# Kernel tuning notes

Measured on AMD Instinct MI355X. Metric: run time of the kernel, lower is better.

Reference implementation:

```python
import jax, jax.numpy as jnp
import numpy as np

N = 1_000_000
HID = 128

def setup_inputs() -> dict:
    key = jax.random.key(0)
    ks = jax.random.split(key, 4)
    F = jnp.eye(2, dtype=jnp.float32)[None] + 0.1 * jax.random.normal(ks[0], (N, 2, 2), dtype=jnp.float32)
    W1 = jax.random.normal(ks[1], (7, HID), dtype=jnp.float32) * (1.0 / np.sqrt(7))
    b1 = jnp.zeros((HID,), dtype=jnp.float32)
    W2 = jax.random.normal(ks[2], (HID, HID), dtype=jnp.float32) * (1.0 / np.sqrt(HID))
    b2 = jnp.zeros((HID,), dtype=jnp.float32)
    W3 = jax.random.normal(ks[3], (HID, 4), dtype=jnp.float32) * (1.0 / np.sqrt(HID))
    b3 = jnp.zeros((4,), dtype=jnp.float32)
    return {"F": F, "W1": W1, "b1": b1, "W2": W2, "b2": b2, "W3": W3, "b3": b3}

def reference(F, W1, b1, W2, b2, W3, b3):
    F = F.reshape(-1, 2, 2)                      # [N,2,2]
    U, sigma, Vh = jnp.linalg.svd(F)             # batched 2x2 SVD
    R = jnp.matmul(U, Vh)                        # rotation part, [N,2,2]
    FtF = jnp.einsum('nij,nik->njk', F, F)       # F^T F, [N,2,2]
    I = jnp.eye(2, dtype=F.dtype)
    I1 = sigma - 1.0                             # [N,2]
    I2 = (FtF - I).reshape(-1, 4)                # [N,4]
    det = F[:, 0, 0] * F[:, 1, 1] - F[:, 0, 1] * F[:, 1, 0]
    I3 = det[:, None] - 1.0                      # [N,1]
    inv = jnp.concatenate([I1, I2, I3], axis=1)  # [N,7]
    h = jax.nn.relu(inv @ W1 + b1)
    h = jax.nn.relu(h @ W2 + b2)
    x = (h @ W3 + b3).reshape(-1, 2, 2)
    x = (x + jnp.swapaxes(x, 1, 2)) * 0.5        # symmetrize
    delta_Fp = jnp.matmul(R, x)
    return delta_Fp + F
```

## Files before the change

kernel.cpp:

```cpp
#include <hip/hip_runtime.h>

typedef _Float16 f16x8 __attribute__((ext_vector_type(8)));
typedef __fp16   fp16x2r __attribute__((ext_vector_type(2)));
typedef float    f32x4 __attribute__((ext_vector_type(4)));

#define MFMA(a, b, c) __builtin_amdgcn_mfma_f32_16x16x32_f16((a), (b), (c), 0, 0, 0)

__device__ inline f16x8 zero8() {
    f16x8 z;
#pragma unroll
    for (int i = 0; i < 8; ++i) z[i] = (_Float16)0.0f;
    return z;
}

__device__ inline f16x8 relu_pack8_rtn(f32x4 lo, f32x4 hi) {
    f16x8 v;
#pragma unroll
    for (int i = 0; i < 4; ++i) {
        v[i]     = (_Float16)fmaxf(lo[i], 0.f);
        v[i + 4] = (_Float16)fmaxf(hi[i], 0.f);
    }
    return v;
}

__device__ inline f16x8 relu_pack8_rtz(f32x4 lo, f32x4 hi) {
    const fp16x2r p0 = __builtin_amdgcn_cvt_pkrtz(fmaxf(lo[0], 0.f), fmaxf(lo[1], 0.f));
    const fp16x2r p1 = __builtin_amdgcn_cvt_pkrtz(fmaxf(lo[2], 0.f), fmaxf(lo[3], 0.f));
    const fp16x2r p2 = __builtin_amdgcn_cvt_pkrtz(fmaxf(hi[0], 0.f), fmaxf(hi[1], 0.f));
    const fp16x2r p3 = __builtin_amdgcn_cvt_pkrtz(fmaxf(hi[2], 0.f), fmaxf(hi[3], 0.f));
    uint4 u = { __builtin_bit_cast(unsigned int, p0), __builtin_bit_cast(unsigned int, p1),
                __builtin_bit_cast(unsigned int, p2), __builtin_bit_cast(unsigned int, p3) };
    return __builtin_bit_cast(f16x8, u);
}

__global__ __launch_bounds__(256, 1)
void DeformationCorrector_78967268704761_kernel(
        const float* __restrict__ F,
        const float* __restrict__ W1, const float* __restrict__ b1,
        const float* __restrict__ W2, const float* __restrict__ b2,
        const float* __restrict__ W3, const float* __restrict__ b3,
        float* __restrict__ out, int N)
{
    __shared__ __align__(16) _Float16 W2A[8][4][64][8];
    __shared__ __align__(16) _Float16 W1A[8][16][8];
    __shared__ __align__(16) _Float16 W3A[4][16][8];
    __shared__ __align__(16) float    b2L[128];
    __shared__ __align__(16) _Float16 invL[4][64][8];

    const int tid  = threadIdx.x;
    const int lane = tid & 63;
    const int w    = tid >> 6;
    const int l15  = tid & 15;
    const int quad = (tid >> 4) & 3;

    for (int m = tid; m < 128 * 128; m += 256) {
        const int k = m >> 7, n = m & 127;
        const int s = k >> 5, j = ((k >> 4) & 1) * 4 + (k & 3), q = (k >> 2) & 3;
        W2A[n >> 4][s][q * 16 + (n & 15)][j] = (_Float16)W2[m];
    }
    for (int f = tid; f < 1024; f += 256) {
        const int mt = f >> 7, n15 = (f >> 3) & 15, j = f & 7;
        W1A[mt][n15][j] = (_Float16)((j < 7) ? W1[j * 128 + mt * 16 + n15]
                                             : b1[mt * 16 + n15]);
    }
    for (int f = tid; f < 512; f += 256) {
        const int s3 = f >> 7, idx = (f >> 3) & 15, j = f & 7;
        const int q = idx >> 2, c3 = idx & 3;
        const int ch2 = (2 * s3 + (j >> 2)) * 16 + q * 4 + (j & 3);
        W3A[s3][idx][j] = (_Float16)W3[ch2 * 4 + c3];
    }
    if (tid < 128) b2L[tid] = b2[tid];
    f32x4 b3i;
    {
        const float4 t = *(const float4*)b3;
        b3i = (quad == 0) ? (f32x4){t.x, t.y, t.z, t.w} : (f32x4){0.f, 0.f, 0.f, 0.f};
    }
    __syncthreads();

    const int ntiles = (N + 255) >> 8;
    const int stride = (int)gridDim.x;

    float a, b, c, d;
    {
        const int p0 = blockIdx.x * 256 + tid;
        if (blockIdx.x < ntiles && p0 < N) {
            const float4 f4 = *(const float4*)(F + 4ll * p0);
            a = f4.x; b = f4.y; c = f4.z; d = f4.w;
        } else { a = 1.f; b = 0.f; c = 0.f; d = 1.f; }
    }

    for (int tile = blockIdx.x; tile < ntiles; tile += stride) {
        float na = 1.f, nb = 0.f, nc = 0.f, nd = 1.f;
        {
            const int pn = (tile + stride) * 256 + tid;
            if (tile + stride < ntiles && pn < N) {
                const float4 f4 = *(const float4*)(F + 4ll * pn);
                na = f4.x; nb = f4.y; nc = f4.z; nd = f4.w;
            }
        }
        const int p = tile * 256 + tid;

        const float x1 = a + d, y1 = c - b, x2 = a - d, y2 = c + b;
        const float h1v = sqrtf(x1 * x1 + y1 * y1);
        const float h2v = sqrtf(x2 * x2 + y2 * y2);
        const float s1 = 0.5f * (h1v + h2v), s2 = 0.5f * (h1v - h2v);
        const float ir = 1.0f / h1v;
        const float Rc = x1 * ir, Rs = y1 * ir;
        f16x8 iv;
        iv[0] = (_Float16)(s1 - 1.f);
        iv[1] = (_Float16)(s2 - 1.f);
        iv[2] = (_Float16)(a * a + c * c - 1.f);
        const float i3 = a * b + c * d;
        iv[3] = (_Float16)i3;
        iv[4] = (_Float16)i3;
        iv[5] = (_Float16)(b * b + d * d - 1.f);
        iv[6] = (_Float16)(a * d - b * c - 1.f);
        iv[7] = (_Float16)1.0f;
        *(f16x8*)(&invL[w][lane][0]) = iv;

        f16x8 B1[4];
#pragma unroll
        for (int nt = 0; nt < 4; ++nt)
            B1[nt] = (quad == 0) ? *(const f16x8*)(&invL[w][nt * 16 + l15][0]) : zero8();

        f16x8 B2[4][4];
#pragma unroll
        for (int s = 0; s < 4; ++s) {
            const f16x8 aLo = (quad == 0) ? *(const f16x8*)(&W1A[2 * s][l15][0])     : zero8();
            const f16x8 aHi = (quad == 0) ? *(const f16x8*)(&W1A[2 * s + 1][l15][0]) : zero8();
#pragma unroll
            for (int nt = 0; nt < 4; ++nt) {
                const f32x4 cz  = {0.f, 0.f, 0.f, 0.f};
                const f32x4 dLo = MFMA(aLo, B1[nt], cz);
                const f32x4 dHi = MFMA(aHi, B1[nt], cz);
                B2[s][nt] = relu_pack8_rtn(dLo, dHi);
            }
        }

        f32x4 acc3[4];
#pragma unroll
        for (int nt = 0; nt < 4; ++nt) acc3[nt] = b3i;

#pragma unroll
        for (int s3 = 0; s3 < 4; ++s3) {
            f32x4 accE[4], accO[4];
            {
                const f32x4 bvE = *(const f32x4*)(&b2L[(2 * s3) * 16 + quad * 4]);
                const f32x4 bvO = *(const f32x4*)(&b2L[(2 * s3 + 1) * 16 + quad * 4]);
#pragma unroll
                for (int nt = 0; nt < 4; ++nt) { accE[nt] = bvE; accO[nt] = bvO; }
            }
#pragma unroll
            for (int s = 0; s < 4; ++s) {
                const f16x8 aE = *(const f16x8*)(&W2A[2 * s3][s][lane][0]);
                const f16x8 aO = *(const f16x8*)(&W2A[2 * s3 + 1][s][lane][0]);
#pragma unroll
                for (int nt = 0; nt < 4; ++nt) {
                    accE[nt] = MFMA(aE, B2[s][nt], accE[nt]);
                    accO[nt] = MFMA(aO, B2[s][nt], accO[nt]);
                }
            }
            const f16x8 a3 = (l15 < 4) ? *(const f16x8*)(&W3A[s3][quad * 4 + l15][0]) : zero8();
#pragma unroll
            for (int nt = 0; nt < 4; ++nt) {
                const f16x8 b3f = relu_pack8_rtz(accE[nt], accO[nt]);
                acc3[nt] = MFMA(a3, b3f, acc3[nt]);
            }
        }

        if (quad == 0) {
#pragma unroll
            for (int nt = 0; nt < 4; ++nt)
                *(f16x8*)(&invL[w][nt * 16 + l15][0]) = __builtin_bit_cast(f16x8, acc3[nt]);
        }
        const f32x4 xv = __builtin_bit_cast(f32x4, *(const f16x8*)(&invL[w][lane][0]));
        const float xm  = 0.5f * (xv[1] + xv[2]);
        const float d00 = Rc * xv[0] - Rs * xm;
        const float d01 = Rc * xm    - Rs * xv[3];
        const float d10 = Rs * xv[0] + Rc * xm;
        const float d11 = Rs * xm    + Rc * xv[3];
        if (p < N) {
            float4 o;
            o.x = a + d00; o.y = b + d01; o.z = c + d10; o.w = d + d11;
            *(float4*)(out + 4ll * p) = o;
        }

        a = na; b = nb; c = nc; d = nd;
    }
}

extern "C" void kernel_launch(void* const* d_in, const int* in_sizes, int n_in,
                              void* d_out, int out_size, void* d_ws, size_t ws_size,
                              hipStream_t stream) {
    const float* F  = (const float*)d_in[0];
    const float* W1 = (const float*)d_in[1];
    const float* b1 = (const float*)d_in[2];
    const float* W2 = (const float*)d_in[3];
    const float* b2 = (const float*)d_in[4];
    const float* W3 = (const float*)d_in[5];
    const float* b3 = (const float*)d_in[6];
    float* out = (float*)d_out;
    const int N = in_sizes[0] / 4;
    const int ntiles = (N + 255) / 256;
    const int grid = ntiles < 512 ? ntiles : 512;
    DeformationCorrector_78967268704761_kernel<<<grid, 256, 0, stream>>>(
        F, W1, b1, W2, b2, W3, b3, out, N);
}
```

Baseline: 141.8 us.

## Process MLP per 16-point subtile in rolled loop and drop F prefetch

The per-wave MLP now loops over the four 16-point column groups with a non-unrolled loop instead of holding all four groups' activations and accumulators in registers at once, and the software prefetch of the next tile's F values is removed. The b3 bias moves into shared memory and is added after the last MFMA. This cuts register pressure, but it also cuts the independent MFMA chains available to hide latency, and W2 fragments are re-read from LDS four times per tile. With launch_bounds(256,1) and a fixed grid, occupancy may not rise, so the lost ILP and the lost load prefetch could dominate.

```diff
diff --git a/kernel.cpp b/kernel.cpp
--- a/kernel.cpp
+++ b/kernel.cpp
@@ -45,6 +45,7 @@
     __shared__ __align__(16) _Float16 W1A[8][16][8];
     __shared__ __align__(16) _Float16 W3A[4][16][8];
     __shared__ __align__(16) float    b2L[128];
+    __shared__ __align__(16) float    b3L[4];
     __shared__ __align__(16) _Float16 invL[4][64][8];
 
     const int tid  = threadIdx.x;
@@ -70,35 +71,20 @@
         W3A[s3][idx][j] = (_Float16)W3[ch2 * 4 + c3];
     }
     if (tid < 128) b2L[tid] = b2[tid];
-    f32x4 b3i;
-    {
-        const float4 t = *(const float4*)b3;
-        b3i = (quad == 0) ? (f32x4){t.x, t.y, t.z, t.w} : (f32x4){0.f, 0.f, 0.f, 0.f};
-    }
+    if (tid < 4)   b3L[tid] = b3[tid];
     __syncthreads();
 
     const int ntiles = (N + 255) >> 8;
     const int stride = (int)gridDim.x;
 
-    float a, b, c, d;
-    {
-        const int p0 = blockIdx.x * 256 + tid;
-        if (blockIdx.x < ntiles && p0 < N) {
-            const float4 f4 = *(const float4*)(F + 4ll * p0);
+    for (int tile = blockIdx.x; tile < ntiles; tile += stride) {
+        const int p = tile * 256 + tid;
+
+        float a, b, c, d;
+        if (p < N) {
+            const float4 f4 = *(const float4*)(F + 4ll * p);
             a = f4.x; b = f4.y; c = f4.z; d = f4.w;
         } else { a = 1.f; b = 0.f; c = 0.f; d = 1.f; }
-    }
-
-    for (int tile = blockIdx.x; tile < ntiles; tile += stride) {
-        float na = 1.f, nb = 0.f, nc = 0.f, nd = 1.f;
-        {
-            const int pn = (tile + stride) * 256 + tid;
-            if (tile + stride < ntiles && pn < N) {
-                const float4 f4 = *(const float4*)(F + 4ll * pn);
-                na = f4.x; nb = f4.y; nc = f4.z; nd = f4.w;
-            }
-        }
-        const int p = tile * 256 + tid;
 
         const float x1 = a + d, y1 = c - b, x2 = a - d, y2 = c + b;
         const float h1v = sqrtf(x1 * x1 + y1 * y1);
@@ -118,61 +104,46 @@
         iv[7] = (_Float16)1.0f;
         *(f16x8*)(&invL[w][lane][0]) = iv;
 
-        f16x8 B1[4];
+#pragma unroll 1
+        for (int q4 = 0; q4 < 4; ++q4) {
+            const f16x8 B1 = (quad == 0)
+                ? *(const f16x8*)(&invL[w][q4 * 16 + l15][0]) : zero8();
+
+            f16x8 B2[4];
 #pragma unroll
-        for (int nt = 0; nt < 4; ++nt)
-            B1[nt] = (quad == 0) ? *(const f16x8*)(&invL[w][nt * 16 + l15][0]) : zero8();
+            for (int s = 0; s < 4; ++s) {
+                const f16x8 aLo = (quad == 0) ? *(const f16x8*)(&W1A[2 * s][l15][0])     : zero8();
+                const f16x8 aHi = (quad == 0) ? *(const f16x8*)(&W1A[2 * s + 1][l15][0]) : zero8();
+                const f32x4 cz  = {0.f, 0.f, 0.f, 0.f};
+                const f32x4 dLo = MFMA(aLo, B1, cz);
+                const f32x4 dHi = MFMA(aHi, B1, cz);
+                B2[s] = relu_pack8_rtn(dLo, dHi);
+            }
 
-        f16x8 B2[4][4];
+            f32x4 acc3 = {0.f, 0.f, 0.f, 0.f};
 #pragma unroll
-        for (int s = 0; s < 4; ++s) {
-            const f16x8 aLo = (quad == 0) ? *(const f16x8*)(&W1A[2 * s][l15][0])     : zero8();
-            const f16x8 aHi = (quad == 0) ? *(const f16x8*)(&W1A[2 * s + 1][l15][0]) : zero8();
+            for (int s3 = 0; s3 < 4; ++s3) {
+                f32x4 accE = *(const f32x4*)(&b2L[(2 * s3) * 16 + quad * 4]);
+                f32x4 accO = *(const f32x4*)(&b2L[(2 * s3 + 1) * 16 + quad * 4]);
 #pragma unroll
-            for (int nt = 0; nt < 4; ++nt) {
-                const f32x4 cz  = {0.f, 0.f, 0.f, 0.f};
-                const f32x4 dLo = MFMA(aLo, B1[nt], cz);
-                const f32x4 dHi = MFMA(aHi, B1[nt], cz);
-                B2[s][nt] = relu_pack8_rtn(dLo, dHi);
+                for (int s = 0; s < 4; ++s) {
+                    const f16x8 aE = *(const f16x8*)(&W2A[2 * s3][s][lane][0]);
+                    const f16x8 aO = *(const f16x8*)(&W2A[2 * s3 + 1][s][lane][0]);
+                    accE = MFMA(aE, B2[s], accE);
+                    accO = MFMA(aO, B2[s], accO);
+                }
+                const f16x8 a3 = (l15 < 4) ? *(const f16x8*)(&W3A[s3][quad * 4 + l15][0]) : zero8();
+                const f16x8 b3f = relu_pack8_rtz(accE, accO);
+                acc3 = MFMA(a3, b3f, acc3);
+            }
+
+            if (quad == 0) {
+                const f32x4 b3v4 = *(const f32x4*)(&b3L[0]);
+                *(f16x8*)(&invL[w][q4 * 16 + l15][0]) =
+                    __builtin_bit_cast(f16x8, acc3 + b3v4);
             }
         }
 
-        f32x4 acc3[4];
-#pragma unroll
-        for (int nt = 0; nt < 4; ++nt) acc3[nt] = b3i;
-
-#pragma unroll
-        for (int s3 = 0; s3 < 4; ++s3) {
-            f32x4 accE[4], accO[4];
-            {
-                const f32x4 bvE = *(const f32x4*)(&b2L[(2 * s3) * 16 + quad * 4]);
-                const f32x4 bvO = *(const f32x4*)(&b2L[(2 * s3 + 1) * 16 + quad * 4]);
-#pragma unroll
-                for (int nt = 0; nt < 4; ++nt) { accE[nt] = bvE; accO[nt] = bvO; }
-            }
-#pragma unroll
-            for (int s = 0; s < 4; ++s) {
-                const f16x8 aE = *(const f16x8*)(&W2A[2 * s3][s][lane][0]);
-                const f16x8 aO = *(const f16x8*)(&W2A[2 * s3 + 1][s][lane][0]);
-#pragma unroll
-                for (int nt = 0; nt < 4; ++nt) {
-                    accE[nt] = MFMA(aE, B2[s][nt], accE[nt]);
-                    accO[nt] = MFMA(aO, B2[s][nt], accO[nt]);
-                }
-            }
-            const f16x8 a3 = (l15 < 4) ? *(const f16x8*)(&W3A[s3][quad * 4 + l15][0]) : zero8();
-#pragma unroll
-            for (int nt = 0; nt < 4; ++nt) {
-                const f16x8 b3f = relu_pack8_rtz(accE[nt], accO[nt]);
-                acc3[nt] = MFMA(a3, b3f, acc3[nt]);
-            }
-        }
-
-        if (quad == 0) {
-#pragma unroll
-            for (int nt = 0; nt < 4; ++nt)
-                *(f16x8*)(&invL[w][nt * 16 + l15][0]) = __builtin_bit_cast(f16x8, acc3[nt]);
-        }
         const f32x4 xv = __builtin_bit_cast(f32x4, *(const f16x8*)(&invL[w][lane][0]));
         const float xm  = 0.5f * (xv[1] + xv[2]);
         const float d00 = Rc * xv[0] - Rs * xm;
@@ -184,8 +155,6 @@
             o.x = a + d00; o.y = b + d01; o.z = c + d10; o.w = d + d11;
             *(float4*)(out + 4ll * p) = o;
         }
-
-        a = na; b = nb; c = nc; d = nd;
     }
 }
 
```

Result: faster. 133.7 us (-5.7%).
